# Optimization experiments

Measured on AMD Instinct MI355X. Metric: run time of the kernel, lower is better.

The kernel has to match this reference:

```python
import jax, jax.numpy as jnp
import numpy as np

GAMMA = 0.99
GAE_LAMBDA = 0.95
CLIP = 0.2
ENT_COEF = 0.01
VF_COEF = 0.5


def setup_inputs() -> dict:
    key = jax.random.key(0)
    ks = jax.random.split(key, 12)
    T, D, H, A = 65536, 512, 256, 16
    obs = jax.random.normal(ks[0], (T, D), dtype=jnp.float32)
    actions = jax.random.randint(ks[1], (T,), 0, A, dtype=jnp.int32)
    logprobs = jax.random.normal(ks[2], (T,), dtype=jnp.float32)
    rewards = jax.random.normal(ks[3], (T,), dtype=jnp.float32)
    terms = jax.random.uniform(ks[4], (T,), dtype=jnp.float32)
    values = jax.random.normal(ks[5], (T,), dtype=jnp.float32)
    # orthogonal-init-like scaling (std sqrt(2) for trunk, 0.01 actor, 1.0 critic)
    W1 = jax.random.normal(ks[6], (D, H), dtype=jnp.float32) * np.float32(np.sqrt(2.0 / D))
    b1 = jnp.zeros((H,), jnp.float32)
    W2 = jax.random.normal(ks[7], (H, H), dtype=jnp.float32) * np.float32(np.sqrt(2.0 / H))
    b2 = jnp.zeros((H,), jnp.float32)
    Wa = jax.random.normal(ks[8], (H, A), dtype=jnp.float32) * np.float32(0.01 / np.sqrt(H))
    ba = jnp.zeros((A,), jnp.float32)
    Wc = jax.random.normal(ks[9], (H, 1), dtype=jnp.float32) * np.float32(1.0 / np.sqrt(H))
    bc = jnp.zeros((1,), jnp.float32)
    return {"obs": obs, "actions": actions, "logprobs": logprobs, "rewards": rewards,
            "terms": terms, "values": values, "W1": W1, "b1": b1, "W2": W2, "b2": b2,
            "Wa": Wa, "ba": ba, "Wc": Wc, "bc": bc}


def reference(obs, actions, logprobs, rewards, terms, values,
              W1, b1, W2, b2, Wa, ba, Wc, bc):
    # ---- GAE (torch.no_grad in original -> stop_gradient) ----
    nonterm = 1.0 - terms                                   # [T]
    next_vals = jnp.concatenate([values[1:], jnp.zeros((1,), values.dtype)])
    delta = rewards + GAMMA * next_vals * nonterm - values  # [T]

    def step(carry, x):  # reverse recurrence a_t = d_t + g*l*nt_t * a_{t+1}
        d, nt = x
        g = d + GAMMA * GAE_LAMBDA * nt * carry
        return g, g

    _, adv = jax.lax.scan(step, jnp.float32(0.0), (delta, nonterm), reverse=True)
    adv = jax.lax.stop_gradient(adv)
    returns = adv + jax.lax.stop_gradient(values)
    vals_old = jax.lax.stop_gradient(values)

    # ---- actor-critic MLP (get_action_and_value) ----
    hidden = jnp.tanh(jnp.tanh(obs @ W1 + b1) @ W2 + b2)    # [T,256]
    logits = hidden @ Wa + ba                               # [T,A]
    logp = jax.nn.log_softmax(logits, axis=-1)
    newlp = jnp.take_along_axis(logp, actions[:, None].astype(jnp.int32), axis=1)[:, 0]
    entropy = -jnp.sum(jnp.exp(logp) * logp, axis=-1)       # [T]
    value = (hidden @ Wc + bc)[:, 0]                        # [T]

    # ---- clipped PPO losses (single full-batch minibatch) ----
    ratio = jnp.exp(newlp - logprobs)
    a = (adv - adv.mean()) / (adv.std() + 1e-8)
    pg_loss = jnp.maximum(-a * ratio, -a * jnp.clip(ratio, 1.0 - CLIP, 1.0 + CLIP)).mean()
    v_clipped = vals_old + jnp.clip(value - vals_old, -CLIP, CLIP)
    v_loss = 0.5 * jnp.maximum((value - returns) ** 2, (v_clipped - returns) ** 2).mean()
    loss = pg_loss - ENT_COEF * entropy.mean() + VF_COEF * v_loss
    return loss
```

## Files before the change

kernel.cpp:

```cpp
#include <hip/hip_runtime.h>


#define TT 65536

typedef float f32x4 __attribute__((ext_vector_type(4)));
typedef __bf16 bf16x8 __attribute__((ext_vector_type(8)));
typedef unsigned short u16x8 __attribute__((ext_vector_type(8)));

__device__ __forceinline__ unsigned short f2bf(float f) {
    unsigned int u = __float_as_uint(f);
    unsigned int r = (u + 0x7fffu + ((u >> 16) & 1u)) >> 16;
    return (unsigned short)r;
}

__device__ __forceinline__ float fast_tanh(float x) {
    float e = __expf(2.0f * x);
    return fmaf(-2.0f, __builtin_amdgcn_rcpf(e + 1.0f), 1.0f);
}

__device__ __forceinline__ void async_lds16(void* lds, const void* g) {
    __builtin_amdgcn_global_load_lds(
        (const __attribute__((address_space(1))) unsigned int*)g,
        (__attribute__((address_space(3))) unsigned int*)lds, 16, 0, 0);
}

__device__ __forceinline__ void suffix_scan256(float* sC, float* sD, int i) {
    float c = sC[i], d = sD[i];
#pragma unroll
    for (int s = 1; s < 256; s <<= 1) {
        float c2 = 1.0f, d2 = 0.0f;
        if (i + s < 256) { c2 = sC[i + s]; d2 = sD[i + s]; }
        __syncthreads();
        d = d + c * d2;
        c = c * c2;
        sC[i] = c; sD[i] = d;
        __syncthreads();
    }
}

__device__ __forceinline__ void gae_cd(const float* rewards, const float* terms,
                                       const float* values, int t, float* c, float* d) {
    float nt = 1.0f - terms[t];
    float nv = (t + 1 < TT) ? values[t + 1] : 0.0f;
    *d = rewards[t] + 0.99f * nv * nt - values[t];
    *c = 0.99f * 0.95f * nt;
}

__global__ void k_prep_gae1(const float* __restrict__ W1, const float* __restrict__ W2,
                            const float* __restrict__ Wa, const float* __restrict__ Wc,
                            unsigned short* __restrict__ W1T, unsigned short* __restrict__ W2T,
                            unsigned short* __restrict__ WavT,
                            const float* __restrict__ rewards, const float* __restrict__ terms,
                            const float* __restrict__ values, float* __restrict__ aggC,
                            float* __restrict__ aggD) {
    if (blockIdx.x < 800) {
        int idx = blockIdx.x * 256 + threadIdx.x;
        if (idx < 131072) {
            int n = idx >> 9, k = idx & 511;
            W1T[idx] = f2bf(W1[k * 256 + n]);
        } else if (idx < 196608) {
            int i = idx - 131072;
            int n = i >> 8, k = i & 255;
            W2T[i] = f2bf(W2[k * 256 + n]);
        } else if (idx < 204800) {
            int i = idx - 196608;
            int r = i >> 8, k = i & 255;
            float v = (r < 16) ? Wa[k * 16 + r] : ((r == 16) ? Wc[k] : 0.0f);
            WavT[i] = f2bf(v);
        }
        return;
    }
    __shared__ float sC[256], sD[256];
    int i = threadIdx.x;
    int b = blockIdx.x - 800;
    int t = b * 256 + i;
    float c, d;
    gae_cd(rewards, terms, values, t, &c, &d);
    sC[i] = c; sD[i] = d;
    __syncthreads();
    suffix_scan256(sC, sD, i);
    if (i == 0) { aggC[b] = sC[0]; aggD[b] = sD[0]; }
}

__global__ void k_gae3(const float* __restrict__ rewards, const float* __restrict__ terms,
                       const float* __restrict__ values, const float* __restrict__ aggC,
                       const float* __restrict__ aggD, float* __restrict__ adv,
                       float* __restrict__ ret, float* __restrict__ sumP) {
    __shared__ float sC[256], sD[256];
    int i = threadIdx.x, b = blockIdx.x;
    sC[i] = aggC[i]; sD[i] = aggD[i];
    __syncthreads();
    suffix_scan256(sC, sD, i);
    float carry = (b < 255) ? sD[b + 1] : 0.0f;
    __syncthreads();

    int t = b * 256 + i;
    float c, d;
    gae_cd(rewards, terms, values, t, &c, &d);
    sC[i] = c; sD[i] = d;
    __syncthreads();
    suffix_scan256(sC, sD, i);
    float a = sD[i] + sC[i] * carry;
    adv[t] = a;
    ret[t] = a + values[t];
    __syncthreads();
    sC[i] = a; sD[i] = a * a;
    __syncthreads();
#pragma unroll
    for (int s = 128; s > 0; s >>= 1) {
        if (i < s) { sC[i] += sC[i + s]; sD[i] += sD[i + s]; }
        __syncthreads();
    }
    if (i == 0) { sumP[2 * b] = sC[0]; sumP[2 * b + 1] = sD[0]; }
}

__global__ void k_gae4(const float* __restrict__ sumP, float* __restrict__ stats) {
    __shared__ float s1[256], s2[256];
    int i = threadIdx.x;
    s1[i] = sumP[2 * i]; s2[i] = sumP[2 * i + 1];
    __syncthreads();
#pragma unroll
    for (int s = 128; s > 0; s >>= 1) {
        if (i < s) { s1[i] += s1[i + s]; s2[i] += s2[i + s]; }
        __syncthreads();
    }
    if (i == 0) {
        float mean = s1[0] * (1.0f / TT);
        float var = s2[0] * (1.0f / TT) - mean * mean;
        float stdv = sqrtf(fmaxf(var, 0.0f));
        stats[0] = mean;
        stats[1] = 1.0f / (stdv + 1e-8f);
    }
}

__global__ __launch_bounds__(256, 2) void k_mlp(
    const float* __restrict__ obs, const int* __restrict__ actions,
    const float* __restrict__ logprobs, const float* __restrict__ values,
    const float* __restrict__ b1, const float* __restrict__ b2,
    const float* __restrict__ ba, const float* __restrict__ bc,
    const unsigned short* __restrict__ W1T, const unsigned short* __restrict__ W2T,
    const unsigned short* __restrict__ WavT, const float* __restrict__ adv,
    const float* __restrict__ ret, const float* __restrict__ stats,
    float* __restrict__ lossP) {
    __shared__ __align__(16) unsigned short smA[64 * 64];
    __shared__ __align__(16) unsigned short smB[256 * 64];
    __shared__ __align__(16) unsigned short smH[64 * 256];
    __shared__ float smRed[4];

    const int tid = threadIdx.x;
    const int wid = tid >> 6;
    const int lane = tid & 63;
    const int cl = lane & 15;
    const int gg = lane >> 4;
    const int bm0 = blockIdx.x * 64;

    float b1v[4], b2v[4];
#pragma unroll
    for (int n = 0; n < 4; ++n) {
        int c = wid * 64 + n * 16 + cl;
        b1v[n] = b1[c];
        b2v[n] = b2[c];
    }
    const float bav = ba[cl];
    const float bc0 = bc[0];
    const float meanA = stats[0], rstdA = stats[1];

    f32x4 acc[4][4];
#pragma unroll
    for (int m = 0; m < 4; ++m)
#pragma unroll
        for (int n = 0; n < 4; ++n) acc[m][n] = (f32x4){0.f, 0.f, 0.f, 0.f};

    const int arow = tid >> 2;
    const int aseg = tid & 3;

    for (int ks = 0; ks < 8; ++ks) {
        const int k0 = ks * 64;
#pragma unroll
        for (int it = 0; it < 8; ++it) {
            int chunk = it * 4 + wid;
            int n = chunk * 8 + (lane >> 3);
            int eoff = 8 * ((lane & 7) ^ (lane >> 3));
            async_lds16(&smB[chunk * 512], W1T + n * 512 + k0 + eoff);
        }
        {
            const float* src = obs + (size_t)(bm0 + arow) * 512 + k0 + aseg * 16;
            float4 f0 = *(const float4*)(src);
            float4 f1 = *(const float4*)(src + 4);
            float4 f2 = *(const float4*)(src + 8);
            float4 f3 = *(const float4*)(src + 12);
            float fv[16];
            *(float4*)&fv[0] = f0; *(float4*)&fv[4] = f1;
            *(float4*)&fv[8] = f2; *(float4*)&fv[12] = f3;
            u16x8 c0, c1;
#pragma unroll
            for (int q = 0; q < 8; ++q) c0[q] = f2bf(fv[q]);
#pragma unroll
            for (int q = 0; q < 8; ++q) c1[q] = f2bf(fv[8 + q]);
            const int msk = (arow & 7) << 3;
            *(u16x8*)&smA[arow * 64 + ((aseg * 16) ^ msk)] = c0;
            *(u16x8*)&smA[arow * 64 + ((aseg * 16 + 8) ^ msk)] = c1;
        }
        __syncthreads();
#pragma unroll
        for (int s = 0; s < 2; ++s) {
            bf16x8 av[4], bv[4];
#pragma unroll
            for (int m = 0; m < 4; ++m) {
                int r = m * 16 + cl;
                av[m] = *(const bf16x8*)&smA[r * 64 + ((s * 32 + gg * 8) ^ ((r & 7) << 3))];
            }
#pragma unroll
            for (int n = 0; n < 4; ++n) {
                int rb = wid * 64 + n * 16 + cl;
                bv[n] = *(const bf16x8*)&smB[rb * 64 + ((s * 32 + gg * 8) ^ ((rb & 7) << 3))];
            }
#pragma unroll
            for (int m = 0; m < 4; ++m)
#pragma unroll
                for (int n = 0; n < 4; ++n)
                    acc[m][n] = __builtin_amdgcn_mfma_f32_16x16x32_bf16(av[m], bv[n], acc[m][n], 0, 0, 0);
        }
        __syncthreads();
    }
#pragma unroll
    for (int m = 0; m < 4; ++m)
#pragma unroll
        for (int n = 0; n < 4; ++n)
#pragma unroll
            for (int j = 0; j < 4; ++j) {
                int r = m * 16 + gg * 4 + j;
                int c = wid * 64 + n * 16 + cl;
                float v = fast_tanh(acc[m][n][j] + b1v[n]);
                smH[r * 256 + (c ^ ((r & 7) << 3))] = f2bf(v);
                acc[m][n][j] = 0.0f;
            }

    for (int ks = 0; ks < 4; ++ks) {
#pragma unroll
        for (int it = 0; it < 8; ++it) {
            int chunk = it * 4 + wid;
            int n = chunk * 8 + (lane >> 3);
            int eoff = 8 * ((lane & 7) ^ (lane >> 3));
            async_lds16(&smB[chunk * 512], W2T + n * 256 + ks * 64 + eoff);
        }
        __syncthreads();
#pragma unroll
        for (int s = 0; s < 2; ++s) {
            bf16x8 av[4], bv[4];
#pragma unroll
            for (int m = 0; m < 4; ++m) {
                int r = m * 16 + cl;
                av[m] = *(const bf16x8*)&smH[r * 256 + ((ks * 64 + s * 32 + gg * 8) ^ ((r & 7) << 3))];
            }
#pragma unroll
            for (int n = 0; n < 4; ++n) {
                int rb = wid * 64 + n * 16 + cl;
                bv[n] = *(const bf16x8*)&smB[rb * 64 + ((s * 32 + gg * 8) ^ ((rb & 7) << 3))];
            }
#pragma unroll
            for (int m = 0; m < 4; ++m)
#pragma unroll
                for (int n = 0; n < 4; ++n)
                    acc[m][n] = __builtin_amdgcn_mfma_f32_16x16x32_bf16(av[m], bv[n], acc[m][n], 0, 0, 0);
        }
        __syncthreads();
    }
#pragma unroll
    for (int m = 0; m < 4; ++m)
#pragma unroll
        for (int n = 0; n < 4; ++n)
#pragma unroll
            for (int j = 0; j < 4; ++j) {
                int r = m * 16 + gg * 4 + j;
                int c = wid * 64 + n * 16 + cl;
                float v = fast_tanh(acc[m][n][j] + b2v[n]);
                smH[r * 256 + (c ^ ((r & 7) << 3))] = f2bf(v);
            }
#pragma unroll
    for (int it = 0; it < 4; ++it) {
        int chunk = it * 4 + wid;
        int n = chunk * 2 + (lane >> 5);
        int e = (lane & 31) * 8;
        async_lds16(&smB[chunk * 512], WavT + n * 256 + (e ^ ((n & 7) << 3)));
    }
    __syncthreads();

    f32x4 acc_a = {0.f, 0.f, 0.f, 0.f}, acc_v = {0.f, 0.f, 0.f, 0.f};
#pragma unroll
    for (int kk = 0; kk < 8; ++kk) {
        int r = wid * 16 + cl;
        bf16x8 av = *(const bf16x8*)&smH[r * 256 + ((kk * 32 + gg * 8) ^ ((r & 7) << 3))];
        int ra = cl;
        bf16x8 bva = *(const bf16x8*)&smB[ra * 256 + ((kk * 32 + gg * 8) ^ ((ra & 7) << 3))];
        int rv = 16 + cl;
        bf16x8 bvv = *(const bf16x8*)&smB[rv * 256 + ((kk * 32 + gg * 8) ^ ((rv & 7) << 3))];
        acc_a = __builtin_amdgcn_mfma_f32_16x16x32_bf16(av, bva, acc_a, 0, 0, 0);
        acc_v = __builtin_amdgcn_mfma_f32_16x16x32_bf16(av, bvv, acc_v, 0, 0, 0);
    }

    float lsum = 0.0f;
    const int t0 = bm0 + wid * 16;
#pragma unroll
    for (int j = 0; j < 4; ++j) {
        int t = t0 + gg * 4 + j;
        float lg = acc_a[j] + bav;
        float mx = lg;
#pragma unroll
        for (int dd = 1; dd < 16; dd <<= 1) mx = fmaxf(mx, __shfl_xor(mx, dd));
        float ex = __expf(lg - mx);
        float se = ex;
#pragma unroll
        for (int dd = 1; dd < 16; dd <<= 1) se += __shfl_xor(se, dd);
        float ls = __logf(se);
        float lp = lg - mx - ls;
        float pl = __expf(lp) * lp;
        float ent = pl;
#pragma unroll
        for (int dd = 1; dd < 16; dd <<= 1) ent += __shfl_xor(ent, dd);
        ent = -ent;
        int act = actions[t];
        float newlp = __shfl(lp, (lane & 48) | act);
        float val = __shfl(acc_v[j], lane & 48) + bc0;

        float lpo = logprobs[t];
        float at = (adv[t] - meanA) * rstdA;
        float rt = ret[t];
        float vo = values[t];
        float ratio = __expf(newlp - lpo);
        float rcl = fminf(fmaxf(ratio, 0.8f), 1.2f);
        float pg = fmaxf(-at * ratio, -at * rcl);
        float vcl = vo + fminf(fmaxf(val - vo, -0.2f), 0.2f);
        float dv = val - rt, dvc = vcl - rt;
        float vl = fmaxf(dv * dv, dvc * dvc);
        if (cl == 0) lsum += pg - 0.01f * ent + 0.25f * vl;
    }
    lsum += __shfl_xor(lsum, 16);
    lsum += __shfl_xor(lsum, 32);
    if (lane == 0) smRed[wid] = lsum;
    __syncthreads();
    if (tid == 0) lossP[blockIdx.x] = smRed[0] + smRed[1] + smRed[2] + smRed[3];
}

__global__ void k_final(const float* __restrict__ lossP, float* __restrict__ out) {
    __shared__ float s[256];
    int i = threadIdx.x;
    s[i] = lossP[i] + lossP[i + 256] + lossP[i + 512] + lossP[i + 768];
    __syncthreads();
#pragma unroll
    for (int st = 128; st > 0; st >>= 1) {
        if (i < st) s[i] += s[i + st];
        __syncthreads();
    }
    if (i == 0) out[0] = s[0] * (1.0f / TT);
}

extern "C" void kernel_launch(void* const* d_in, const int* in_sizes, int n_in,
                              void* d_out, int out_size, void* d_ws, size_t ws_size,
                              hipStream_t stream) {
    const float* obs      = (const float*)d_in[0];
    const int*   actions  = (const int*)d_in[1];
    const float* logprobs = (const float*)d_in[2];
    const float* rewards  = (const float*)d_in[3];
    const float* terms    = (const float*)d_in[4];
    const float* values   = (const float*)d_in[5];
    const float* W1 = (const float*)d_in[6];
    const float* b1 = (const float*)d_in[7];
    const float* W2 = (const float*)d_in[8];
    const float* b2 = (const float*)d_in[9];
    const float* Wa = (const float*)d_in[10];
    const float* ba = (const float*)d_in[11];
    const float* Wc = (const float*)d_in[12];
    const float* bc = (const float*)d_in[13];

    char* ws = (char*)d_ws;
    unsigned short* W1T  = (unsigned short*)(ws + 0);
    unsigned short* W2T  = (unsigned short*)(ws + 262144);
    unsigned short* WavT = (unsigned short*)(ws + 393216);
    float* advp  = (float*)(ws + 409600);
    float* retp  = (float*)(ws + 671744);
    float* aggC  = (float*)(ws + 933888);
    float* aggD  = (float*)(ws + 934912);
    float* sumP  = (float*)(ws + 936960);
    float* stats = (float*)(ws + 939008);
    float* lossP = (float*)(ws + 939072);

    k_prep_gae1<<<1056, 256, 0, stream>>>(W1, W2, Wa, Wc, W1T, W2T, WavT,
                                          rewards, terms, values, aggC, aggD);
    k_gae3<<<256, 256, 0, stream>>>(rewards, terms, values, aggC, aggD, advp, retp, sumP);
    k_gae4<<<1, 256, 0, stream>>>(sumP, stats);
    k_mlp<<<1024, 256, 0, stream>>>(obs, actions, logprobs, values, b1, b2, ba, bc,
                                    W1T, W2T, WavT, advp, retp, stats, lossP);
    k_final<<<1, 256, 0, stream>>>(lossP, (float*)d_out);
}
```

Before: 67.39 us.

## Double-buffer MLP GEMM tiles and fold advantage-stats reduction into MLP kernel

Restructures the layer-1 and layer-2 GEMM loops to use K=32 double-buffered LDS tiles. The next weight tile is prefetched asynchronously and the next obs tile is loaded into registers while the current tile feeds the MFMAs, which leaves one barrier per step instead of two. The separate single-block k_gae4 launch is removed, and every MLP block now reduces the 256 partial sums itself to get the mean and std. This saves a launch and a serial dependency but adds redundant reduction work in each of the 1024 blocks.

```diff
diff --git a/kernel.cpp b/kernel.cpp
--- a/kernel.cpp
+++ b/kernel.cpp
@@ -114,25 +114,6 @@
     if (i == 0) { sumP[2 * b] = sC[0]; sumP[2 * b + 1] = sD[0]; }
 }
 
-__global__ void k_gae4(const float* __restrict__ sumP, float* __restrict__ stats) {
-    __shared__ float s1[256], s2[256];
-    int i = threadIdx.x;
-    s1[i] = sumP[2 * i]; s2[i] = sumP[2 * i + 1];
-    __syncthreads();
-#pragma unroll
-    for (int s = 128; s > 0; s >>= 1) {
-        if (i < s) { s1[i] += s1[i + s]; s2[i] += s2[i + s]; }
-        __syncthreads();
-    }
-    if (i == 0) {
-        float mean = s1[0] * (1.0f / TT);
-        float var = s2[0] * (1.0f / TT) - mean * mean;
-        float stdv = sqrtf(fmaxf(var, 0.0f));
-        stats[0] = mean;
-        stats[1] = 1.0f / (stdv + 1e-8f);
-    }
-}
-
 __global__ __launch_bounds__(256, 2) void k_mlp(
     const float* __restrict__ obs, const int* __restrict__ actions,
     const float* __restrict__ logprobs, const float* __restrict__ values,
@@ -140,10 +121,10 @@
     const float* __restrict__ ba, const float* __restrict__ bc,
     const unsigned short* __restrict__ W1T, const unsigned short* __restrict__ W2T,
     const unsigned short* __restrict__ WavT, const float* __restrict__ adv,
-    const float* __restrict__ ret, const float* __restrict__ stats,
+    const float* __restrict__ ret, const float* __restrict__ sumP,
     float* __restrict__ lossP) {
-    __shared__ __align__(16) unsigned short smA[64 * 64];
-    __shared__ __align__(16) unsigned short smB[256 * 64];
+    __shared__ __align__(16) unsigned short smA[2][64 * 32];
+    __shared__ __align__(16) unsigned short smB[2][256 * 32];
     __shared__ __align__(16) unsigned short smH[64 * 256];
     __shared__ float smRed[4];
 
@@ -154,6 +135,23 @@
     const int gg = lane >> 4;
     const int bm0 = blockIdx.x * 64;
 
+    float meanA, rstdA;
+    {
+        float* red = (float*)smH;
+        red[tid] = sumP[2 * tid];
+        red[256 + tid] = sumP[2 * tid + 1];
+        __syncthreads();
+#pragma unroll
+        for (int s = 128; s > 0; s >>= 1) {
+            if (tid < s) { red[tid] += red[tid + s]; red[256 + tid] += red[256 + tid + s]; }
+            __syncthreads();
+        }
+        meanA = red[0] * (1.0f / TT);
+        float var = red[256] * (1.0f / TT) - meanA * meanA;
+        rstdA = 1.0f / (sqrtf(fmaxf(var, 0.0f)) + 1e-8f);
+        __syncthreads();
+    }
+
     float b1v[4], b2v[4];
 #pragma unroll
     for (int n = 0; n < 4; ++n) {
@@ -163,7 +161,6 @@
     }
     const float bav = ba[cl];
     const float bc0 = bc[0];
-    const float meanA = stats[0], rstdA = stats[1];
 
     f32x4 acc[4][4];
 #pragma unroll
@@ -172,57 +169,84 @@
         for (int n = 0; n < 4; ++n) acc[m][n] = (f32x4){0.f, 0.f, 0.f, 0.f};
 
     const int arow = tid >> 2;
-    const int aseg = tid & 3;
-
-    for (int ks = 0; ks < 8; ++ks) {
-        const int k0 = ks * 64;
-#pragma unroll
-        for (int it = 0; it < 8; ++it) {
+    const int akoff = ((tid & 3) ^ ((arow >> 1) & 3)) << 3;
+    const float* aptr = obs + (size_t)(bm0 + arow) * 512 + akoff;
+
+    float4 pa[2][2];
+
+    auto stageB1 = [&](int t1) {
+        const int k0 = t1 * 32;
+#pragma unroll
+        for (int it = 0; it < 4; ++it) {
             int chunk = it * 4 + wid;
-            int n = chunk * 8 + (lane >> 3);
-            int eoff = 8 * ((lane & 7) ^ (lane >> 3));
-            async_lds16(&smB[chunk * 512], W1T + n * 512 + k0 + eoff);
-        }
-        {
-            const float* src = obs + (size_t)(bm0 + arow) * 512 + k0 + aseg * 16;
-            float4 f0 = *(const float4*)(src);
-            float4 f1 = *(const float4*)(src + 4);
-            float4 f2 = *(const float4*)(src + 8);
-            float4 f3 = *(const float4*)(src + 12);
-            float fv[16];
-            *(float4*)&fv[0] = f0; *(float4*)&fv[4] = f1;
-            *(float4*)&fv[8] = f2; *(float4*)&fv[12] = f3;
-            u16x8 c0, c1;
-#pragma unroll
-            for (int q = 0; q < 8; ++q) c0[q] = f2bf(fv[q]);
-#pragma unroll
-            for (int q = 0; q < 8; ++q) c1[q] = f2bf(fv[8 + q]);
-            const int msk = (arow & 7) << 3;
-            *(u16x8*)&smA[arow * 64 + ((aseg * 16) ^ msk)] = c0;
-            *(u16x8*)&smA[arow * 64 + ((aseg * 16 + 8) ^ msk)] = c1;
-        }
-        __syncthreads();
-#pragma unroll
-        for (int s = 0; s < 2; ++s) {
-            bf16x8 av[4], bv[4];
-#pragma unroll
-            for (int m = 0; m < 4; ++m) {
-                int r = m * 16 + cl;
-                av[m] = *(const bf16x8*)&smA[r * 64 + ((s * 32 + gg * 8) ^ ((r & 7) << 3))];
-            }
-#pragma unroll
-            for (int n = 0; n < 4; ++n) {
-                int rb = wid * 64 + n * 16 + cl;
-                bv[n] = *(const bf16x8*)&smB[rb * 64 + ((s * 32 + gg * 8) ^ ((rb & 7) << 3))];
-            }
-#pragma unroll
-            for (int m = 0; m < 4; ++m)
-#pragma unroll
-                for (int n = 0; n < 4; ++n)
-                    acc[m][n] = __builtin_amdgcn_mfma_f32_16x16x32_bf16(av[m], bv[n], acc[m][n], 0, 0, 0);
-        }
-        __syncthreads();
-    }
+            int row = chunk * 16 + (lane >> 2);
+            int koff = ((lane & 3) ^ ((row >> 1) & 3)) << 3;
+            async_lds16(&smB[t1 & 1][chunk * 512], W1T + row * 512 + k0 + koff);
+        }
+    };
+    auto stageB2 = [&](int t1) {
+        const int k0 = t1 * 32;
+#pragma unroll
+        for (int it = 0; it < 4; ++it) {
+            int chunk = it * 4 + wid;
+            int row = chunk * 16 + (lane >> 2);
+            int koff = ((lane & 3) ^ ((row >> 1) & 3)) << 3;
+            async_lds16(&smB[t1 & 1][chunk * 512], W2T + row * 256 + k0 + koff);
+        }
+    };
+    auto stageWav = [&]() {
+#pragma unroll
+        for (int it = 0; it < 4; ++it) {
+            int chunk = it * 4 + wid;
+            int L = chunk * 64 + lane;
+            int row = L >> 5;
+            int e = (L & 31) * 8;
+            async_lds16(&smB[0][chunk * 512], WavT + row * 256 + (e ^ ((row & 7) << 3)));
+        }
+    };
+    auto loadA = [&](int t, float4* dst) {
+        dst[0] = *(const float4*)(aptr + t * 32);
+        dst[1] = *(const float4*)(aptr + t * 32 + 4);
+    };
+    auto convA = [&](const float4* src, int buf) {
+        u16x8 cc;
+        cc[0] = f2bf(src[0].x); cc[1] = f2bf(src[0].y);
+        cc[2] = f2bf(src[0].z); cc[3] = f2bf(src[0].w);
+        cc[4] = f2bf(src[1].x); cc[5] = f2bf(src[1].y);
+        cc[6] = f2bf(src[1].z); cc[7] = f2bf(src[1].w);
+        *(u16x8*)&smA[buf][tid * 8] = cc;
+    };
+
+    stageB1(0);
+    loadA(0, pa[0]);
+    loadA(1, pa[1]);
+    convA(pa[0], 0);
+    __syncthreads();
+
+#pragma unroll
+    for (int t = 0; t < 16; ++t) {
+        if (t < 15) stageB1(t + 1); else stageB2(0);
+        if (t < 14) loadA(t + 2, pa[t & 1]);
+        if (t < 15) convA(pa[(t + 1) & 1], (t + 1) & 1);
+        bf16x8 av[4], bv[4];
+#pragma unroll
+        for (int m = 0; m < 4; ++m) {
+            int ra = m * 16 + cl;
+            av[m] = *(const bf16x8*)&smA[t & 1][ra * 32 + (((gg ^ ((ra >> 1) & 3))) << 3)];
+        }
+#pragma unroll
+        for (int n = 0; n < 4; ++n) {
+            int rb = wid * 64 + n * 16 + cl;
+            bv[n] = *(const bf16x8*)&smB[t & 1][rb * 32 + (((gg ^ ((rb >> 1) & 3))) << 3)];
+        }
+#pragma unroll
+        for (int m = 0; m < 4; ++m)
+#pragma unroll
+            for (int n = 0; n < 4; ++n)
+                acc[m][n] = __builtin_amdgcn_mfma_f32_16x16x32_bf16(av[m], bv[n], acc[m][n], 0, 0, 0);
+        __syncthreads();
+    }
+
 #pragma unroll
     for (int m = 0; m < 4; ++m)
 #pragma unroll
@@ -235,37 +259,30 @@
                 smH[r * 256 + (c ^ ((r & 7) << 3))] = f2bf(v);
                 acc[m][n][j] = 0.0f;
             }
-
-    for (int ks = 0; ks < 4; ++ks) {
-#pragma unroll
-        for (int it = 0; it < 8; ++it) {
-            int chunk = it * 4 + wid;
-            int n = chunk * 8 + (lane >> 3);
-            int eoff = 8 * ((lane & 7) ^ (lane >> 3));
-            async_lds16(&smB[chunk * 512], W2T + n * 256 + ks * 64 + eoff);
-        }
-        __syncthreads();
-#pragma unroll
-        for (int s = 0; s < 2; ++s) {
-            bf16x8 av[4], bv[4];
-#pragma unroll
-            for (int m = 0; m < 4; ++m) {
-                int r = m * 16 + cl;
-                av[m] = *(const bf16x8*)&smH[r * 256 + ((ks * 64 + s * 32 + gg * 8) ^ ((r & 7) << 3))];
-            }
-#pragma unroll
-            for (int n = 0; n < 4; ++n) {
-                int rb = wid * 64 + n * 16 + cl;
-                bv[n] = *(const bf16x8*)&smB[rb * 64 + ((s * 32 + gg * 8) ^ ((rb & 7) << 3))];
-            }
-#pragma unroll
-            for (int m = 0; m < 4; ++m)
-#pragma unroll
-                for (int n = 0; n < 4; ++n)
-                    acc[m][n] = __builtin_amdgcn_mfma_f32_16x16x32_bf16(av[m], bv[n], acc[m][n], 0, 0, 0);
-        }
-        __syncthreads();
-    }
+    __syncthreads();
+
+#pragma unroll
+    for (int t = 0; t < 8; ++t) {
+        if (t < 7) stageB2(t + 1); else stageWav();
+        bf16x8 av[4], bv[4];
+#pragma unroll
+        for (int m = 0; m < 4; ++m) {
+            int ra = m * 16 + cl;
+            av[m] = *(const bf16x8*)&smH[ra * 256 + ((t * 32 + gg * 8) ^ ((ra & 7) << 3))];
+        }
+#pragma unroll
+        for (int n = 0; n < 4; ++n) {
+            int rb = wid * 64 + n * 16 + cl;
+            bv[n] = *(const bf16x8*)&smB[t & 1][rb * 32 + (((gg ^ ((rb >> 1) & 3))) << 3)];
+        }
+#pragma unroll
+        for (int m = 0; m < 4; ++m)
+#pragma unroll
+            for (int n = 0; n < 4; ++n)
+                acc[m][n] = __builtin_amdgcn_mfma_f32_16x16x32_bf16(av[m], bv[n], acc[m][n], 0, 0, 0);
+        __syncthreads();
+    }
+
 #pragma unroll
     for (int m = 0; m < 4; ++m)
 #pragma unroll
@@ -277,13 +294,6 @@
                 float v = fast_tanh(acc[m][n][j] + b2v[n]);
                 smH[r * 256 + (c ^ ((r & 7) << 3))] = f2bf(v);
             }
-#pragma unroll
-    for (int it = 0; it < 4; ++it) {
-        int chunk = it * 4 + wid;
-        int n = chunk * 2 + (lane >> 5);
-        int e = (lane & 31) * 8;
-        async_lds16(&smB[chunk * 512], WavT + n * 256 + (e ^ ((n & 7) << 3)));
-    }
     __syncthreads();
 
     f32x4 acc_a = {0.f, 0.f, 0.f, 0.f}, acc_v = {0.f, 0.f, 0.f, 0.f};
@@ -292,9 +302,9 @@
         int r = wid * 16 + cl;
         bf16x8 av = *(const bf16x8*)&smH[r * 256 + ((kk * 32 + gg * 8) ^ ((r & 7) << 3))];
         int ra = cl;
-        bf16x8 bva = *(const bf16x8*)&smB[ra * 256 + ((kk * 32 + gg * 8) ^ ((ra & 7) << 3))];
+        bf16x8 bva = *(const bf16x8*)&smB[0][ra * 256 + ((kk * 32 + gg * 8) ^ ((ra & 7) << 3))];
         int rv = 16 + cl;
-        bf16x8 bvv = *(const bf16x8*)&smB[rv * 256 + ((kk * 32 + gg * 8) ^ ((rv & 7) << 3))];
+        bf16x8 bvv = *(const bf16x8*)&smB[0][rv * 256 + ((kk * 32 + gg * 8) ^ ((rv & 7) << 3))];
         acc_a = __builtin_amdgcn_mfma_f32_16x16x32_bf16(av, bva, acc_a, 0, 0, 0);
         acc_v = __builtin_amdgcn_mfma_f32_16x16x32_bf16(av, bvv, acc_v, 0, 0, 0);
     }
@@ -382,14 +392,12 @@
     float* aggC  = (float*)(ws + 933888);
     float* aggD  = (float*)(ws + 934912);
     float* sumP  = (float*)(ws + 936960);
-    float* stats = (float*)(ws + 939008);
     float* lossP = (float*)(ws + 939072);
 
     k_prep_gae1<<<1056, 256, 0, stream>>>(W1, W2, Wa, Wc, W1T, W2T, WavT,
                                           rewards, terms, values, aggC, aggD);
     k_gae3<<<256, 256, 0, stream>>>(rewards, terms, values, aggC, aggD, advp, retp, sumP);
-    k_gae4<<<1, 256, 0, stream>>>(sumP, stats);
     k_mlp<<<1024, 256, 0, stream>>>(obs, actions, logprobs, values, b1, b2, ba, bc,
-                                    W1T, W2T, WavT, advp, retp, stats, lossP);
+                                    W1T, W2T, WavT, advp, retp, sumP, lossP);
     k_final<<<1, 256, 0, stream>>>(lossP, (float*)d_out);
 }
```

Measured after the change: 70.57 us. 1.05x slower.
